# Optimization experiments

Hardware: AMD Instinct MI355X
Metric: run time of the kernel (lower is better)

Reference implementation:

```python
import jax, jax.numpy as jnp
import numpy as np

R = 5          # number of rating values (relations)
U = 100000     # num users (user_in_units, one-hot ids)
M = 50000      # num items (movie_in_units)
E = 2000000    # edges per rating etype
F = 10         # internal feature dim (hardcoded in module)
D = 50         # per-relation msg dim = msg_units // R = 250 // 5


def setup_inputs() -> dict:
    key = jax.random.key(0)
    ks = jax.random.split(key, 12)
    f = lambda k, shape: jax.random.normal(k, shape, dtype=jnp.float32) * 0.1
    return {
        "edges_src": jax.random.randint(ks[0], (R, E), 0, U, dtype=jnp.int32),  # user endpoint
        "edges_dst": jax.random.randint(ks[1], (R, E), 0, M, dtype=jnp.int32),  # item endpoint
        # per-rating learned node-feature tables (feat1/feat2 of each GCMCGraphSage)
        "feat_u_fwd": f(ks[2], (R, U, F)),  # src feats for user->item conv
        "feat_i_fwd": f(ks[3], (R, M, F)),  # dst feats for user->item conv
        "feat_i_rev": f(ks[4], (R, M, F)),  # src feats for item->user (rev) conv
        "feat_u_rev": f(ks[5], (R, U, F)),  # dst feats for item->user (rev) conv
        # SAGEConv weights per relation (fc_self, fc_neigh, bias)
        "w_self_fwd": f(ks[6], (R, F, D)),
        "w_neigh_fwd": f(ks[7], (R, F, D)),
        "b_fwd": jnp.zeros((R, D), jnp.float32),
        "w_self_rev": f(ks[8], (R, F, D)),
        "w_neigh_rev": f(ks[9], (R, F, D)),
        "b_rev": jnp.zeros((R, D), jnp.float32),
    }


def _sage(feat_src, feat_dst, src, dst, w_self, w_neigh, b, n_dst):
    """DGL SAGEConv 'mean' on a bipartite relation: h = fc_self(x_dst) + fc_neigh(mean_j x_src[j]) + b."""
    msg = feat_src[src]                                               # (E, F) irregular gather
    s = jax.ops.segment_sum(msg, dst, num_segments=n_dst)             # (n_dst, F) scatter-add
    cnt = jax.ops.segment_sum(jnp.ones_like(dst, dtype=feat_src.dtype), dst, num_segments=n_dst)
    h_neigh = s / jnp.maximum(cnt, 1.0)[:, None]                      # zero in-degree -> 0 (DGL mean)
    return feat_dst @ w_self + h_neigh @ w_neigh + b


def reference(edges_src, edges_dst, feat_u_fwd, feat_i_fwd, feat_i_rev, feat_u_rev,
              w_self_fwd, w_neigh_fwd, b_fwd, w_self_rev, w_neigh_rev, b_rev):
    # rating etype: user -> item
    item_per = jax.vmap(lambda fs, fd, s, d, ws, wn, b: _sage(fs, fd, s, d, ws, wn, b, M))(
        feat_u_fwd, feat_i_fwd, edges_src, edges_dst, w_self_fwd, w_neigh_fwd, b_fwd)  # (R, M, D)
    # rev-rating etype: item -> user (edge direction reversed)
    user_per = jax.vmap(lambda fs, fd, s, d, ws, wn, b: _sage(fs, fd, s, d, ws, wn, b, U))(
        feat_i_rev, feat_u_rev, edges_dst, edges_src, w_self_rev, w_neigh_rev, b_rev)  # (R, U, D)
    # HeteroGraphConv aggregate='stack' -> (N, R, D); layer then flattens to (N, R*D)
    ufeat = jnp.transpose(user_per, (1, 0, 2)).reshape(U, R * D)
    ifeat = jnp.transpose(item_per, (1, 0, 2)).reshape(M, R * D)
    return (ufeat, ifeat)
```

## Files before the change

kernel.cpp:

```cpp
#include <hip/hip_runtime.h>

#define R 5
#define U 100000
#define M 50000
#define E 2000000
#define F 10
#define D 50

#define TE (R * E)
#define NBLK 256
#define CHUNK ((TE + NBLK - 1) / NBLK)
#define BSZ 256

#define NKEY 128
#define KS_U (R * U)
#define KS_I (R * M)
#define NBU_U ((KS_U + NKEY - 1) / NKEY)
#define NBU_I ((KS_I + NKEY - 1) / NKEY)
#define NBU_T (NBU_U + NBU_I)
#define OFFI (NBU_U * NBLK)
#define GTOT (OFFI + NBU_I * NBLK)
#define NS1 ((GTOT + 1023) / 1024)
#define S2K ((NS1 + 255) / 256)

#define CAP 6656
#define ASTR 11


__global__ __launch_bounds__(BSZ) void phaseA(const int* __restrict__ esrc,
                                              const int* __restrict__ edst,
                                              unsigned* __restrict__ ghist) {
    __shared__ unsigned hist[NBU_T];
    for (int i = threadIdx.x; i < NBU_T; i += BSZ) hist[i] = 0;
    __syncthreads();
    int b = blockIdx.x;
    int lo = b * CHUNK, hi = min(lo + CHUNK, TE);
    for (int i = lo + threadIdx.x; i < hi; i += BSZ) {
        unsigned r = (unsigned)i / (unsigned)E;
        int s = esrc[i], d = edst[i];
        unsigned ku = r * U + (unsigned)s;
        unsigned ki = r * M + (unsigned)d;
        atomicAdd(&hist[ku >> 7], 1u);
        atomicAdd(&hist[NBU_U + (ki >> 7)], 1u);
    }
    __syncthreads();
    for (int j = threadIdx.x; j < NBU_T; j += BSZ) {
        unsigned idx = (j < NBU_U) ? (unsigned)j * NBLK + b
                                   : OFFI + (unsigned)(j - NBU_U) * NBLK + b;
        ghist[idx] = hist[j];
    }
}

__global__ __launch_bounds__(BSZ) void scan1(unsigned* __restrict__ S,
                                             unsigned* __restrict__ psum) {
    __shared__ unsigned sh[BSZ];
    int base = blockIdx.x * 1024 + threadIdx.x * 4;
    unsigned v[4], tsum = 0;
    for (int k = 0; k < 4; k++) {
        int i = base + k;
        v[k] = (i < GTOT) ? S[i] : 0u;
        tsum += v[k];
    }
    sh[threadIdx.x] = tsum;
    __syncthreads();
    for (int off = 1; off < BSZ; off <<= 1) {
        unsigned t = (threadIdx.x >= off) ? sh[threadIdx.x - off] : 0u;
        __syncthreads();
        sh[threadIdx.x] += t;
        __syncthreads();
    }
    unsigned ex = sh[threadIdx.x] - tsum;
    for (int k = 0; k < 4; k++) {
        int i = base + k;
        if (i < GTOT) S[i] = ex;
        ex += v[k];
    }
    if (threadIdx.x == BSZ - 1) psum[blockIdx.x] = sh[BSZ - 1];
}

__global__ __launch_bounds__(BSZ) void scan2(unsigned* __restrict__ psum) {
    __shared__ unsigned sh[BSZ];
    unsigned v[S2K], tsum = 0;
    int base = threadIdx.x * S2K;
    for (int k = 0; k < S2K; k++) {
        int i = base + k;
        v[k] = (i < NS1) ? psum[i] : 0u;
        tsum += v[k];
    }
    sh[threadIdx.x] = tsum;
    __syncthreads();
    for (int off = 1; off < BSZ; off <<= 1) {
        unsigned t = (threadIdx.x >= off) ? sh[threadIdx.x - off] : 0u;
        __syncthreads();
        sh[threadIdx.x] += t;
        __syncthreads();
    }
    unsigned ex = sh[threadIdx.x] - tsum;
    for (int k = 0; k < S2K; k++) {
        int i = base + k;
        if (i < NS1) psum[i] = ex;
        ex += v[k];
    }
}

__global__ __launch_bounds__(BSZ) void scan3(unsigned* __restrict__ S,
                                             const unsigned* __restrict__ psum) {
    unsigned add = psum[blockIdx.x];
    int base = blockIdx.x * 1024 + threadIdx.x * 4;
    for (int k = 0; k < 4; k++) {
        int i = base + k;
        if (i < GTOT) S[i] += add;
    }
}

__global__ __launch_bounds__(BSZ) void phaseC(const int* __restrict__ esrc,
                                              const int* __restrict__ edst,
                                              const unsigned* __restrict__ S,
                                              unsigned* __restrict__ sorted) {
    __shared__ unsigned cur[NBU_T];
    int b = blockIdx.x;
    for (int j = threadIdx.x; j < NBU_T; j += BSZ) {
        unsigned idx = (j < NBU_U) ? (unsigned)j * NBLK + b
                                   : OFFI + (unsigned)(j - NBU_U) * NBLK + b;
        cur[j] = S[idx];
    }
    __syncthreads();
    int lo = b * CHUNK, hi = min(lo + CHUNK, TE);
    for (int i = lo + threadIdx.x; i < hi; i += BSZ) {
        unsigned r = (unsigned)i / (unsigned)E;
        int s = esrc[i], d = edst[i];
        unsigned ku = r * U + (unsigned)s;
        unsigned ki = r * M + (unsigned)d;
        unsigned pu = atomicAdd(&cur[ku >> 7], 1u);
        sorted[pu] = (ku & 127u) | ((unsigned)d << 7);
        unsigned pi = atomicAdd(&cur[NBU_U + (ki >> 7)], 1u);
        sorted[pi] = (ki & 127u) | ((unsigned)s << 7);
    }
}

__global__ __launch_bounds__(BSZ) void phaseD(
    const unsigned* __restrict__ sorted, const unsigned* __restrict__ S,
    const float* __restrict__ fsrc_u, const float* __restrict__ fdst_u,
    const float* __restrict__ wsf_u, const float* __restrict__ wnf_u,
    const float* __restrict__ bia_u,
    const float* __restrict__ fsrc_i, const float* __restrict__ fdst_i,
    const float* __restrict__ wsf_i, const float* __restrict__ wnf_i,
    const float* __restrict__ bia_i,
    float* __restrict__ out_u, float* __restrict__ out_i) {
    __shared__ unsigned sbuf[CAP];
    __shared__ float acc[NKEY * ASTR];
    __shared__ unsigned hist[NKEY];
    __shared__ unsigned cur[NKEY];
    __shared__ unsigned rbase[NKEY];

    unsigned orig = blockIdx.x;
    unsigned bkt;
    if (orig < NBU_U) {
        const unsigned q = NBU_U / 8u, rem = NBU_U % 8u;
        unsigned x = orig & 7u, off = orig >> 3;
        bkt = (x < rem ? x * (q + 1u) : rem * (q + 1u) + (x - rem) * q) + off;
    } else {
        unsigned o = orig - NBU_U;
        const unsigned q = NBU_I / 8u, rem = NBU_I % 8u;
        unsigned x = o & 7u, off = o >> 3;
        bkt = NBU_U + (x < rem ? x * (q + 1u) : rem * (q + 1u) + (x - rem) * q) + off;
    }

    bool isU = bkt < NBU_U;
    int j = isU ? (int)bkt : (int)bkt - NBU_U;
    unsigned N = isU ? U : M;
    unsigned NSRC = isU ? M : U;
    const float* fsrc = isU ? fsrc_u : fsrc_i;

    unsigned sbase = isU ? 0u : (unsigned)OFFI;
    unsigned lo = S[sbase + (unsigned)j * NBLK];
    unsigned hi = (!isU && j + 1 == NBU_I) ? (unsigned)(2 * TE)
                                           : S[sbase + (unsigned)(j + 1) * NBLK];
    unsigned len = hi - lo;
    unsigned keybase = (unsigned)j * NKEY;
    int tid = threadIdx.x;

    for (int t = tid; t < NKEY * ASTR; t += BSZ) acc[t] = 0.f;
    if (tid < NKEY) {
        hist[tid] = 0u;
        unsigned key = keybase + (unsigned)tid;
        unsigned r = (key < (unsigned)R * N) ? key / N : 0u;
        rbase[tid] = r * NSRC;
    }
    __syncthreads();

    if (len <= CAP) {
        for (unsigned e = lo + tid; e < hi; e += BSZ)
            atomicAdd(&hist[sorted[e] & 127u], 1u);
        __syncthreads();
        if (tid < NKEY) cur[tid] = hist[tid];
        __syncthreads();
        for (int off = 1; off < NKEY; off <<= 1) {
            unsigned t = 0;
            if (tid < NKEY && tid >= off) t = cur[tid - off];
            __syncthreads();
            if (tid < NKEY && tid >= off) cur[tid] += t;
            __syncthreads();
        }
        if (tid < NKEY) cur[tid] -= hist[tid];
        __syncthreads();
        for (unsigned e = lo + tid; e < hi; e += BSZ) {
            unsigned pay = sorted[e];
            unsigned pos = atomicAdd(&cur[pay & 127u], 1u);
            sbuf[pos] = pay;
        }
        __syncthreads();
        unsigned L = (len + BSZ - 1) / BSZ;
        unsigned i0 = (unsigned)tid * L;
        unsigned i1 = min(i0 + L, len);
        if (i0 < i1) {
            int curKey = -1;
            float A0 = 0, A1 = 0, A2 = 0, A3 = 0, A4 = 0,
                  A5 = 0, A6 = 0, A7 = 0, A8 = 0, A9 = 0;
#define FLUSH_ACC()                                                        \
    do {                                                                   \
        if (curKey >= 0) {                                                 \
            float* ap = acc + curKey * ASTR;                               \
            atomicAdd(ap + 0, A0); atomicAdd(ap + 1, A1);                  \
            atomicAdd(ap + 2, A2); atomicAdd(ap + 3, A3);                  \
            atomicAdd(ap + 4, A4); atomicAdd(ap + 5, A5);                  \
            atomicAdd(ap + 6, A6); atomicAdd(ap + 7, A7);                  \
            atomicAdd(ap + 8, A8); atomicAdd(ap + 9, A9);                  \
        }                                                                  \
    } while (0)
#define ZERO_ACC() A0=A1=A2=A3=A4=A5=A6=A7=A8=A9=0.f
            unsigned i = i0;
            for (; i + 1 < i1; i += 2) {
                unsigned p0 = sbuf[i], p1 = sbuf[i + 1];
                unsigned k0 = p0 & 127u, s0 = p0 >> 7;
                unsigned k1 = p1 & 127u, s1 = p1 >> 7;
                const float2* r0 = (const float2*)(fsrc + (size_t)(rbase[k0] + s0) * F);
                const float2* r1 = (const float2*)(fsrc + (size_t)(rbase[k1] + s1) * F);
                float2 x0 = r0[0], x1 = r0[1], x2 = r0[2], x3 = r0[3], x4 = r0[4];
                float2 y0 = r1[0], y1 = r1[1], y2 = r1[2], y3 = r1[3], y4 = r1[4];
                if ((int)k0 != curKey) { FLUSH_ACC(); curKey = (int)k0; ZERO_ACC(); }
                A0 += x0.x; A1 += x0.y; A2 += x1.x; A3 += x1.y; A4 += x2.x;
                A5 += x2.y; A6 += x3.x; A7 += x3.y; A8 += x4.x; A9 += x4.y;
                if ((int)k1 != curKey) { FLUSH_ACC(); curKey = (int)k1; ZERO_ACC(); }
                A0 += y0.x; A1 += y0.y; A2 += y1.x; A3 += y1.y; A4 += y2.x;
                A5 += y2.y; A6 += y3.x; A7 += y3.y; A8 += y4.x; A9 += y4.y;
            }
            if (i < i1) {
                unsigned p0 = sbuf[i];
                unsigned k0 = p0 & 127u, s0 = p0 >> 7;
                const float2* r0 = (const float2*)(fsrc + (size_t)(rbase[k0] + s0) * F);
                float2 x0 = r0[0], x1 = r0[1], x2 = r0[2], x3 = r0[3], x4 = r0[4];
                if ((int)k0 != curKey) { FLUSH_ACC(); curKey = (int)k0; ZERO_ACC(); }
                A0 += x0.x; A1 += x0.y; A2 += x1.x; A3 += x1.y; A4 += x2.x;
                A5 += x2.y; A6 += x3.x; A7 += x3.y; A8 += x4.x; A9 += x4.y;
            }
            FLUSH_ACC();
#undef FLUSH_ACC
#undef ZERO_ACC
        }
    } else {
        for (unsigned e = lo + tid; e < hi; e += BSZ) {
            unsigned pay = sorted[e];
            unsigned l = pay & 127u, s = pay >> 7;
            const float2* row = (const float2*)(fsrc + (size_t)(rbase[l] + s) * F);
            float* a = acc + l * ASTR;
#pragma unroll
            for (int k = 0; k < 5; k++) {
                float2 v = row[k];
                atomicAdd(a + 2 * k, v.x);
                atomicAdd(a + 2 * k + 1, v.y);
            }
            atomicAdd(&hist[l], 1u);
        }
    }
    __syncthreads();

    const float* fdst = isU ? fdst_u : fdst_i;
    const float* wsf = isU ? wsf_u : wsf_i;
    const float* wnf = isU ? wnf_u : wnf_i;
    const float* bia = isU ? bia_u : bia_i;
    float* out = isU ? out_u : out_i;

    for (int o = tid; o < NKEY * D; o += BSZ) {
        int local = o / D, d = o - local * D;
        unsigned key = keybase + (unsigned)local;
        if (key >= (unsigned)(R)*N) continue;
        unsigned r = key / N, n = key - r * N;
        float inv = 1.f / fmaxf((float)hist[local], 1.f);
        const float* fd = fdst + ((size_t)r * N + n) * F;
        const float* a = acc + local * ASTR;
        const float* wsp = wsf + (size_t)r * F * D + d;
        const float* wnp = wnf + (size_t)r * F * D + d;
        float o1 = bia[r * D + d], o2 = 0.f;
#pragma unroll
        for (int f = 0; f < F; f++) {
            o1 += fd[f] * wsp[(size_t)f * D];
            o2 += a[f] * wnp[(size_t)f * D];
        }
        out[(size_t)n * (R * D) + r * D + d] = o1 + o2 * inv;
    }
}

#define SUM_I_OFF 0
#define CNT_I_OFF ((size_t)R * M * F)
#define SUM_U_OFF (CNT_I_OFF + (size_t)R * M)
#define CNT_U_OFF (SUM_U_OFF + (size_t)R * U * F)
#define WS_FLOATS (CNT_U_OFF + (size_t)R * U)

__global__ void scatter_edges(const int* __restrict__ esrc, const int* __restrict__ edst,
                              const float* __restrict__ feat_u_fwd,
                              const float* __restrict__ feat_i_rev, float* __restrict__ ws) {
    float* sum_i = ws + SUM_I_OFF;
    float* cnt_i = ws + CNT_I_OFF;
    float* sum_u = ws + SUM_U_OFF;
    float* cnt_u = ws + CNT_U_OFF;
    const int total = R * E;
    for (int idx = blockIdx.x * blockDim.x + threadIdx.x; idx < total;
         idx += gridDim.x * blockDim.x) {
        int r = idx / E;
        int s = esrc[idx], d = edst[idx];
        const float* fu = feat_u_fwd + ((size_t)r * U + s) * F;
        const float* fi = feat_i_rev + ((size_t)r * M + d) * F;
        float* si = sum_i + ((size_t)r * M + d) * F;
        float* su = sum_u + ((size_t)r * U + s) * F;
#pragma unroll
        for (int f = 0; f < F; ++f) {
            atomicAdd(si + f, fu[f]);
            atomicAdd(su + f, fi[f]);
        }
        atomicAdd(cnt_i + (size_t)r * M + d, 1.0f);
        atomicAdd(cnt_u + (size_t)r * U + s, 1.0f);
    }
}

__global__ void finalize_nodes(int N, const float* __restrict__ feat_dst,
                               const float* __restrict__ w_self, const float* __restrict__ w_neigh,
                               const float* __restrict__ bias, const float* __restrict__ sum,
                               const float* __restrict__ cnt, float* __restrict__ out) {
    int idx = blockIdx.x * blockDim.x + threadIdx.x;
    int total = N * R * D;
    if (idx >= total) return;
    int n = idx / (R * D);
    int rd = idx - n * (R * D);
    int r = rd / D;
    int d = rd - r * D;
    const float* fd = feat_dst + ((size_t)r * N + n) * F;
    const float* sn = sum + ((size_t)r * N + n) * F;
    float inv = 1.0f / fmaxf(cnt[(size_t)r * N + n], 1.0f);
    const float* wsp = w_self + (size_t)r * F * D + d;
    const float* wnp = w_neigh + (size_t)r * F * D + d;
    float acc_self = bias[r * D + d];
    float acc_n = 0.0f;
#pragma unroll
    for (int f = 0; f < F; ++f) {
        acc_self += fd[f] * wsp[(size_t)f * D];
        acc_n += sn[f] * wnp[(size_t)f * D];
    }
    out[idx] = acc_self + acc_n * inv;
}

extern "C" void kernel_launch(void* const* d_in, const int* in_sizes, int n_in,
                              void* d_out, int out_size, void* d_ws, size_t ws_size,
                              hipStream_t stream) {
    const int* edges_src = (const int*)d_in[0];
    const int* edges_dst = (const int*)d_in[1];
    const float* feat_u_fwd = (const float*)d_in[2];
    const float* feat_i_fwd = (const float*)d_in[3];
    const float* feat_i_rev = (const float*)d_in[4];
    const float* feat_u_rev = (const float*)d_in[5];
    const float* w_self_fwd = (const float*)d_in[6];
    const float* w_neigh_fwd = (const float*)d_in[7];
    const float* b_fwd = (const float*)d_in[8];
    const float* w_self_rev = (const float*)d_in[9];
    const float* w_neigh_rev = (const float*)d_in[10];
    const float* b_rev = (const float*)d_in[11];

    float* out = (float*)d_out;
    float* out_u = out;
    float* out_i = out + (size_t)U * R * D;

    size_t need = ((size_t)2 * TE + (size_t)GTOT + 2048ull) * 4ull;
    if (ws_size >= need) {
        unsigned* sorted = (unsigned*)d_ws;
        unsigned* S = sorted + (size_t)2 * TE;
        unsigned* psum = S + GTOT;

        phaseA<<<NBLK, BSZ, 0, stream>>>(edges_src, edges_dst, S);
        scan1<<<NS1, BSZ, 0, stream>>>(S, psum);
        scan2<<<1, BSZ, 0, stream>>>(psum);
        scan3<<<NS1, BSZ, 0, stream>>>(S, psum);
        phaseC<<<NBLK, BSZ, 0, stream>>>(edges_src, edges_dst, S, sorted);
        phaseD<<<NBU_T, BSZ, 0, stream>>>(sorted, S,
                                          feat_i_rev, feat_u_rev, w_self_rev, w_neigh_rev, b_rev,
                                          feat_u_fwd, feat_i_fwd, w_self_fwd, w_neigh_fwd, b_fwd,
                                          out_u, out_i);
    } else {
        float* ws = (float*)d_ws;
        hipMemsetAsync(d_ws, 0, WS_FLOATS * sizeof(float), stream);
        scatter_edges<<<4096, 256, 0, stream>>>(edges_src, edges_dst, feat_u_fwd, feat_i_rev, ws);
        finalize_nodes<<<(U * R * D + 255) / 256, 256, 0, stream>>>(
            U, feat_u_rev, w_self_rev, w_neigh_rev, b_rev, ws + SUM_U_OFF, ws + CNT_U_OFF, out_u);
        finalize_nodes<<<(M * R * D + 255) / 256, 256, 0, stream>>>(
            M, feat_i_fwd, w_self_fwd, w_neigh_fwd, b_fwd, ws + SUM_I_OFF, ws + CNT_I_OFF, out_i);
    }
}
```

Before: 717.5 us.

## Use smaller item buckets, fewer sort blocks, and halve phaseD shared buffer

Splits the bucket width so item keys use 64-key buckets while user keys keep 128, which balances per-block edge counts (about 13k edges per bucket on both sides). Halves the per-bucket shared staging buffer (CAP) and adds a launch-bounds occupancy hint so more phaseD blocks fit per CU. The histogram and scatter passes now use 192 chunks instead of 256, which shrinks the global histogram and scan work. The risk is that buckets larger than the smaller CAP fall back to the slower atomic path, and the item payload loses one bit of headroom.

```diff
diff --git a/kernel.cpp b/kernel.cpp
--- a/kernel.cpp
+++ b/kernel.cpp
@@ -8,22 +8,23 @@
 #define D 50
 
 #define TE (R * E)
-#define NBLK 256
+#define NBLK 192
 #define CHUNK ((TE + NBLK - 1) / NBLK)
 #define BSZ 256
 
-#define NKEY 128
+#define NKEY_U 128
+#define NKEY_I 64
 #define KS_U (R * U)
 #define KS_I (R * M)
-#define NBU_U ((KS_U + NKEY - 1) / NKEY)
-#define NBU_I ((KS_I + NKEY - 1) / NKEY)
+#define NBU_U ((KS_U + NKEY_U - 1) / NKEY_U)
+#define NBU_I ((KS_I + NKEY_I - 1) / NKEY_I)
 #define NBU_T (NBU_U + NBU_I)
 #define OFFI (NBU_U * NBLK)
 #define GTOT (OFFI + NBU_I * NBLK)
 #define NS1 ((GTOT + 1023) / 1024)
 #define S2K ((NS1 + 255) / 256)
 
-#define CAP 6656
+#define CAP 3328
 #define ASTR 11
 
 
@@ -41,7 +42,7 @@
         unsigned ku = r * U + (unsigned)s;
         unsigned ki = r * M + (unsigned)d;
         atomicAdd(&hist[ku >> 7], 1u);
-        atomicAdd(&hist[NBU_U + (ki >> 7)], 1u);
+        atomicAdd(&hist[NBU_U + (ki >> 6)], 1u);
     }
     __syncthreads();
     for (int j = threadIdx.x; j < NBU_T; j += BSZ) {
@@ -133,12 +134,12 @@
         unsigned ki = r * M + (unsigned)d;
         unsigned pu = atomicAdd(&cur[ku >> 7], 1u);
         sorted[pu] = (ku & 127u) | ((unsigned)d << 7);
-        unsigned pi = atomicAdd(&cur[NBU_U + (ki >> 7)], 1u);
-        sorted[pi] = (ki & 127u) | ((unsigned)s << 7);
-    }
-}
-
-__global__ __launch_bounds__(BSZ) void phaseD(
+        unsigned pi = atomicAdd(&cur[NBU_U + (ki >> 6)], 1u);
+        sorted[pi] = (ki & 63u) | ((unsigned)s << 6);
+    }
+}
+
+__global__ __launch_bounds__(BSZ, 8) void phaseD(
     const unsigned* __restrict__ sorted, const unsigned* __restrict__ S,
     const float* __restrict__ fsrc_u, const float* __restrict__ fdst_u,
     const float* __restrict__ wsf_u, const float* __restrict__ wnf_u,
@@ -148,28 +149,28 @@
     const float* __restrict__ bia_i,
     float* __restrict__ out_u, float* __restrict__ out_i) {
     __shared__ unsigned sbuf[CAP];
-    __shared__ float acc[NKEY * ASTR];
-    __shared__ unsigned hist[NKEY];
-    __shared__ unsigned cur[NKEY];
-    __shared__ unsigned rbase[NKEY];
+    __shared__ float acc[NKEY_U * ASTR];
+    __shared__ unsigned hist[NKEY_U];
+    __shared__ unsigned cur[NKEY_U];
+    __shared__ unsigned rbase[NKEY_U];
 
     unsigned orig = blockIdx.x;
     unsigned bkt;
-    if (orig < NBU_U) {
+    {
+        unsigned o = (orig < NBU_U) ? orig : orig - NBU_U;
         const unsigned q = NBU_U / 8u, rem = NBU_U % 8u;
-        unsigned x = orig & 7u, off = orig >> 3;
-        bkt = (x < rem ? x * (q + 1u) : rem * (q + 1u) + (x - rem) * q) + off;
-    } else {
-        unsigned o = orig - NBU_U;
-        const unsigned q = NBU_I / 8u, rem = NBU_I % 8u;
         unsigned x = o & 7u, off = o >> 3;
-        bkt = NBU_U + (x < rem ? x * (q + 1u) : rem * (q + 1u) + (x - rem) * q) + off;
+        unsigned m = (x < rem ? x * (q + 1u) : rem * (q + 1u) + (x - rem) * q) + off;
+        bkt = (orig < NBU_U) ? m : NBU_U + m;
     }
 
     bool isU = bkt < NBU_U;
     int j = isU ? (int)bkt : (int)bkt - NBU_U;
     unsigned N = isU ? U : M;
     unsigned NSRC = isU ? M : U;
+    unsigned NKEY = isU ? NKEY_U : NKEY_I;
+    unsigned KM = NKEY - 1u;
+    unsigned KSH = isU ? 7u : 6u;
     const float* fsrc = isU ? fsrc_u : fsrc_i;
 
     unsigned sbase = isU ? 0u : (unsigned)OFFI;
@@ -180,8 +181,8 @@
     unsigned keybase = (unsigned)j * NKEY;
     int tid = threadIdx.x;
 
-    for (int t = tid; t < NKEY * ASTR; t += BSZ) acc[t] = 0.f;
-    if (tid < NKEY) {
+    for (int t = tid; t < NKEY_U * ASTR; t += BSZ) acc[t] = 0.f;
+    if (tid < NKEY_U) {
         hist[tid] = 0u;
         unsigned key = keybase + (unsigned)tid;
         unsigned r = (key < (unsigned)R * N) ? key / N : 0u;
@@ -191,22 +192,22 @@
 
     if (len <= CAP) {
         for (unsigned e = lo + tid; e < hi; e += BSZ)
-            atomicAdd(&hist[sorted[e] & 127u], 1u);
-        __syncthreads();
-        if (tid < NKEY) cur[tid] = hist[tid];
-        __syncthreads();
-        for (int off = 1; off < NKEY; off <<= 1) {
+            atomicAdd(&hist[sorted[e] & KM], 1u);
+        __syncthreads();
+        if (tid < NKEY_U) cur[tid] = hist[tid];
+        __syncthreads();
+        for (int off = 1; off < NKEY_U; off <<= 1) {
             unsigned t = 0;
-            if (tid < NKEY && tid >= off) t = cur[tid - off];
+            if (tid < NKEY_U && tid >= off) t = cur[tid - off];
             __syncthreads();
-            if (tid < NKEY && tid >= off) cur[tid] += t;
+            if (tid < NKEY_U && tid >= off) cur[tid] += t;
             __syncthreads();
         }
-        if (tid < NKEY) cur[tid] -= hist[tid];
+        if (tid < NKEY_U) cur[tid] -= hist[tid];
         __syncthreads();
         for (unsigned e = lo + tid; e < hi; e += BSZ) {
             unsigned pay = sorted[e];
-            unsigned pos = atomicAdd(&cur[pay & 127u], 1u);
+            unsigned pos = atomicAdd(&cur[pay & KM], 1u);
             sbuf[pos] = pay;
         }
         __syncthreads();
@@ -232,8 +233,8 @@
             unsigned i = i0;
             for (; i + 1 < i1; i += 2) {
                 unsigned p0 = sbuf[i], p1 = sbuf[i + 1];
-                unsigned k0 = p0 & 127u, s0 = p0 >> 7;
-                unsigned k1 = p1 & 127u, s1 = p1 >> 7;
+                unsigned k0 = p0 & KM, s0 = p0 >> KSH;
+                unsigned k1 = p1 & KM, s1 = p1 >> KSH;
                 const float2* r0 = (const float2*)(fsrc + (size_t)(rbase[k0] + s0) * F);
                 const float2* r1 = (const float2*)(fsrc + (size_t)(rbase[k1] + s1) * F);
                 float2 x0 = r0[0], x1 = r0[1], x2 = r0[2], x3 = r0[3], x4 = r0[4];
@@ -247,7 +248,7 @@
             }
             if (i < i1) {
                 unsigned p0 = sbuf[i];
-                unsigned k0 = p0 & 127u, s0 = p0 >> 7;
+                unsigned k0 = p0 & KM, s0 = p0 >> KSH;
                 const float2* r0 = (const float2*)(fsrc + (size_t)(rbase[k0] + s0) * F);
                 float2 x0 = r0[0], x1 = r0[1], x2 = r0[2], x3 = r0[3], x4 = r0[4];
                 if ((int)k0 != curKey) { FLUSH_ACC(); curKey = (int)k0; ZERO_ACC(); }
@@ -261,7 +262,7 @@
     } else {
         for (unsigned e = lo + tid; e < hi; e += BSZ) {
             unsigned pay = sorted[e];
-            unsigned l = pay & 127u, s = pay >> 7;
+            unsigned l = pay & KM, s = pay >> KSH;
             const float2* row = (const float2*)(fsrc + (size_t)(rbase[l] + s) * F);
             float* a = acc + l * ASTR;
 #pragma unroll
@@ -281,7 +282,8 @@
     const float* bia = isU ? bia_u : bia_i;
     float* out = isU ? out_u : out_i;
 
-    for (int o = tid; o < NKEY * D; o += BSZ) {
+    int tot = (int)NKEY * D;
+    for (int o = tid; o < tot; o += BSZ) {
         int local = o / D, d = o - local * D;
         unsigned key = keybase + (unsigned)local;
         if (key >= (unsigned)(R)*N) continue;
```

After: 742.6 us. 3.5% more time.
